# Kernel optimization log

Measured on AMD Instinct MI355X. Metric: run time of the kernel, lower is better.

Reference implementation:

```python
import jax, jax.numpy as jnp
import numpy as np

H, D = 8, 8          # num_heads, hidden_size (head dim)
SCALE = 0.25         # Hopfield beta/scaling
STEPS = 3            # update_steps_max
LN_EPS = 1e-5


def ln(x, g, b):
    m = x.mean(-1, keepdims=True)
    v = ((x - m) ** 2).mean(-1, keepdims=True)
    return (x - m) * jax.lax.rsqrt(v + LN_EPS) * g + b


def setup_inputs() -> dict:
    key = jax.random.key(0)
    ks = jax.random.split(key, 8)
    B, N, E = 32, 512, 512
    P = H * D  # 64 virtual hopfield dim
    s = lambda k, shape: jax.random.normal(k, shape, jnp.float32) * 0.05
    return dict(
        x=jax.random.normal(ks[0], (B, N, E), jnp.float32),
        g_q=jnp.ones((E,), jnp.float32), b_q=jnp.zeros((E,), jnp.float32),
        g_k=jnp.ones((E,), jnp.float32), b_k=jnp.zeros((E,), jnp.float32),
        g_v=jnp.ones((E,), jnp.float32), b_v=jnp.zeros((E,), jnp.float32),
        Wq=s(ks[1], (P, E)), bq=jnp.zeros((P,), jnp.float32),
        Wk=s(ks[2], (P, E)), bk=jnp.zeros((P,), jnp.float32),
        Wv=s(ks[3], (P, E)), bv=jnp.zeros((P,), jnp.float32),
        Wo=s(ks[4], (E, P)), bo=jnp.zeros((E,), jnp.float32),
        Wl=s(ks[5], (1, N * E)), bl=jnp.zeros((1,), jnp.float32),
    )


def reference(x, g_q, b_q, g_k, b_k, g_v, b_v,
              Wq, bq, Wk, bk, Wv, bv, Wo, bo, Wl, bl):
    B, N, E = x.shape
    # LayerNorm on state (query), stored (key), projection (value) patterns
    q = (ln(x, g_q, b_q) @ Wq.T + bq).reshape(B, N, H, D)
    k = (ln(x, g_k, b_k) @ Wk.T + bk).reshape(B, N, H, D)
    v = (ln(x, g_v, b_v) @ Wv.T + bv).reshape(B, N, H, D)
    # iterative Hopfield retrieval: xi <- softmax(beta * xi K^T) K
    xi = q
    for _ in range(STEPS):
        a = jax.nn.softmax(SCALE * jnp.einsum('bihd,bjhd->bhij', xi, k), axis=-1)
        xi = jnp.einsum('bhij,bjhd->bihd', a, k)
    # final association with value patterns
    a = jax.nn.softmax(SCALE * jnp.einsum('bihd,bjhd->bhij', xi, k), axis=-1)
    o = jnp.einsum('bhij,bjhd->bihd', a, v).reshape(B, N, H * D)
    o = o @ Wo.T + bo              # (B, N, E) out projection
    y = o.reshape(B, N * E) @ Wl.T + bl  # (B, 1) classifier head
    return y.reshape(-1)           # flatten(start_dim=0) -> (B,)
```

## Files before the change

### kernel.cpp

```cpp
#include <hip/hip_runtime.h>

#define E_DIM 512
#define N_DIM 512
#define B_DIM 32
#define H_DIM 8
#define D_DIM 8
#define P3    192

typedef _Float16 half_t;
typedef __attribute__((ext_vector_type(2))) _Float16 half2v;
typedef __attribute__((ext_vector_type(4))) _Float16 half4v;
typedef __attribute__((ext_vector_type(8))) _Float16 half8v;
typedef __attribute__((ext_vector_type(4))) float f32x4;
typedef __attribute__((ext_vector_type(16))) float f32x16;
typedef __attribute__((ext_vector_type(2))) unsigned int u32x2;
typedef __attribute__((ext_vector_type(4))) unsigned int u32x4;

#define XS_STRIDE 520
#define CQ 0.3606737602222409f
#define LS_RS 136

#define SM_KT0 0
#define SM_VT0 4608
#define SM_KB0 9216
#define SM_TOT 13312

__device__ inline float block_reduce_256(float v) {
    __shared__ float red[4];
    #pragma unroll
    for (int m = 32; m >= 1; m >>= 1) v += __shfl_xor(v, m);
    int w = threadIdx.x >> 6;
    if ((threadIdx.x & 63) == 0) red[w] = v;
    __syncthreads();
    if (threadIdx.x == 0) v = red[0] + red[1] + red[2] + red[3];
    return v;
}

__device__ inline half8v cvt8(float4 a, float4 b) {
    half8v h;
    h[0] = (half_t)a.x; h[1] = (half_t)a.y; h[2] = (half_t)a.z; h[3] = (half_t)a.w;
    h[4] = (half_t)b.x; h[5] = (half_t)b.y; h[6] = (half_t)b.z; h[7] = (half_t)b.w;
    return h;
}

__device__ inline unsigned pku(float a, float b) {
    return __builtin_bit_cast(unsigned, __builtin_amdgcn_cvt_pkrtz(a, b));
}

__device__ inline void plswap(unsigned &a, unsigned &b) {
    u32x2 r = __builtin_amdgcn_permlane32_swap(a, b, false, false);
    a = r[0]; b = r[1];
}

__device__ inline float bcast_lo(float v) {
    unsigned u = __builtin_bit_cast(unsigned, v);
    u32x2 r = __builtin_amdgcn_permlane32_swap(u, u, false, false);
    return __builtin_bit_cast(float, r[0]);
}

__global__ __launch_bounds__(256) void prep_w(const float* __restrict__ Wq,
                        const float* __restrict__ Wk, const float* __restrict__ Wv,
                        const float* __restrict__ gq, const float* __restrict__ gk,
                        const float* __restrict__ gv,
                        const float* __restrict__ bnq, const float* __restrict__ bnk,
                        const float* __restrict__ bnv,
                        const float* __restrict__ bq, const float* __restrict__ bk,
                        const float* __restrict__ bv,
                        const float* __restrict__ bl,
                        half_t* __restrict__ WthF, float* __restrict__ colsum,
                        float* __restrict__ b2, float* __restrict__ y,
                        float* __restrict__ c0acc) {
    int pp = blockIdx.x;
    int which = pp >> 6, p = pp & 63;
    int ct = pp >> 4, c16 = pp & 15;
    const float* W  = (which == 0) ? Wq  : (which == 1) ? Wk  : Wv;
    const float* g  = (which == 0) ? gq  : (which == 1) ? gk  : gv;
    const float* bn = (which == 0) ? bnq : (which == 1) ? bnk : bnv;
    const float* bb = (which == 0) ? bq  : (which == 1) ? bk  : bv;
    int t = threadIdx.x;
    if (pp == 0) {
        if (t < 32) y[t] = bl[0];
        if (t == 32) c0acc[0] = 0.f;
    }
    float cs = 0.f, dt = 0.f;
    #pragma unroll
    for (int l = 0; l < 2; ++l) {
        int e = t + l * 256;
        float wv = W[p * E_DIM + e];
        half_t wh = (half_t)(wv * g[e]);
        int k32 = e >> 5, g2 = (e >> 3) & 3, j = e & 7;
        WthF[(((size_t)(ct * 16 + k32) * 64) + g2 * 16 + c16) * 8 + j] = wh;
        cs += (float)wh;
        dt += wv * bn[e];
    }
    cs = block_reduce_256(cs);
    __syncthreads();
    dt = block_reduce_256(dt);
    if (t == 0) { colsum[pp] = cs; b2[pp] = dt + bb[p]; }
}

__global__ __launch_bounds__(256) void ln_qkv_wl2(const float* __restrict__ x,
                                              const half_t* __restrict__ WthF,
                                              const float* __restrict__ b2,
                                              const float* __restrict__ colsum,
                                              half_t* __restrict__ qkv16,
                                              const float* __restrict__ Wl,
                                              const float* __restrict__ Wo,
                                              const float* __restrict__ bo,
                                              float* __restrict__ Wl2,
                                              float* __restrict__ c0acc) {
    __shared__ half_t Xs[16 * XS_STRIDE];
    __shared__ half_t Ls[24 * LS_RS];
    __shared__ float stats[16][2];
    if (blockIdx.x < 1024) {
        const int t = threadIdx.x;
        const int lane = t & 63;
        const int w = t >> 6;
        const int g2 = lane >> 4, c16 = lane & 15;
        const int row0 = blockIdx.x * 16;
        {
            const int row = t >> 4, c = t & 15;
            const float4* xrow = (const float4*)(x + (size_t)(row0 + row) * E_DIM);
            float sx = 0.f, sxx = 0.f;
            #pragma unroll
            for (int l = 0; l < 8; ++l) {
                int f4 = c + l * 16;
                float4 a = xrow[f4];
                sx  += a.x + a.y + a.z + a.w;
                sxx += a.x*a.x + a.y*a.y + a.z*a.z + a.w*a.w;
                half4v h;
                h[0] = (half_t)a.x; h[1] = (half_t)a.y;
                h[2] = (half_t)a.z; h[3] = (half_t)a.w;
                *(half4v*)&Xs[row * XS_STRIDE + f4 * 4] = h;
            }
            #pragma unroll
            for (int m = 1; m <= 8; m <<= 1) {
                sx += __shfl_xor(sx, m); sxx += __shfl_xor(sxx, m);
            }
            if (c == 0) {
                float mean = sx * (1.f / E_DIM);
                float var  = sxx * (1.f / E_DIM) - mean * mean;
                stats[row][0] = mean;
                stats[row][1] = rsqrtf(var + 1e-5f);
            }
        }
        __syncthreads();
        f32x4 acc[3] = {{0.f,0.f,0.f,0.f},{0.f,0.f,0.f,0.f},{0.f,0.f,0.f,0.f}};
        const half_t* wf = WthF + (size_t)w * 3 * 16 * 512;
        #pragma unroll 4
        for (int k32 = 0; k32 < 16; ++k32) {
            half8v af = *(const half8v*)&Xs[c16 * XS_STRIDE + k32 * 32 + g2 * 8];
            #pragma unroll
            for (int nt = 0; nt < 3; ++nt) {
                half8v bf = *(const half8v*)(wf + ((size_t)(nt * 16 + k32)) * 512 + lane * 8);
                acc[nt] = __builtin_amdgcn_mfma_f32_16x16x32_f16(af, bf, acc[nt], 0, 0, 0);
            }
        }
        #pragma unroll
        for (int nt = 0; nt < 3; ++nt) {
            int pp = w * 48 + nt * 16 + c16;
            float cs = colsum[pp], bb = b2[pp];
            float qsc = (pp < 64) ? CQ : 1.0f;
            int region = pp >> 3, d = pp & 7;
            #pragma unroll
            for (int r = 0; r < 4; ++r) {
                int rowi = g2 * 4 + r;
                float val = (stats[rowi][1] * (acc[nt][r] - stats[rowi][0] * cs) + bb) * qsc;
                Ls[region * LS_RS + rowi * 8 + d] = (half_t)val;
            }
        }
        __syncthreads();
        const int b = row0 >> 9, n0 = row0 & 511;
        #pragma unroll
        for (int l = 0; l < 3; ++l) {
            int c = t + l * 256;
            int region = c >> 5, off = (c & 31) * 4;
            int which = region >> 3, h = region & 7;
            half4v v = *(const half4v*)&Ls[region * LS_RS + off];
            half_t* dst0 = qkv16 + (size_t)which * (B_DIM * H_DIM * N_DIM * D_DIM);
            int rowi = off >> 3, d0 = off & 7;
            *(half4v*)&dst0[(((size_t)(b * H_DIM + h)) * N_DIM + n0 + rowi) * D_DIM + d0] = v;
        }
    } else {
        const int blk = blockIdx.x - 1024;
        const int t = threadIdx.x;
        const int lane = t & 63;
        const int w = t >> 6;
        const int g2 = lane >> 4, c16 = lane & 15;
        const int n0 = blk * 16;
        const int pcol = w * 16;
        f32x4 acc = {0.f, 0.f, 0.f, 0.f};
        float pc = 0.f;
        const float* arow = Wl + (size_t)(n0 + c16) * E_DIM;
        #pragma unroll 2
        for (int k0 = 0; k0 < E_DIM; k0 += 32) {
            int kbase = k0 + g2 * 8;
            float4 a0 = *(const float4*)(arow + kbase);
            float4 a1 = *(const float4*)(arow + kbase + 4);
            if (w == 0) {
                float4 b0 = *(const float4*)(bo + kbase);
                float4 b1 = *(const float4*)(bo + kbase + 4);
                pc += a0.x*b0.x + a0.y*b0.y + a0.z*b0.z + a0.w*b0.w
                    + a1.x*b1.x + a1.y*b1.y + a1.z*b1.z + a1.w*b1.w;
            }
            half8v af = cvt8(a0, a1);
            half8v bf;
            #pragma unroll
            for (int j = 0; j < 8; ++j)
                bf[j] = (half_t)Wo[(size_t)(kbase + j) * 64 + pcol + c16];
            acc = __builtin_amdgcn_mfma_f32_16x16x32_f16(af, bf, acc, 0, 0, 0);
        }
        int p = pcol + c16, h = p >> 3, d = p & 7;
        #pragma unroll
        for (int r = 0; r < 4; ++r) {
            int n = n0 + g2 * 4 + r;
            Wl2[h * (N_DIM * D_DIM) + n * D_DIM + d] = acc[r];
        }
        if (w == 0) {
            pc += __shfl_xor(pc, 16); pc += __shfl_xor(pc, 32);
            pc += __shfl_xor(pc, 1);  pc += __shfl_xor(pc, 2);
            pc += __shfl_xor(pc, 4);  pc += __shfl_xor(pc, 8);
            if (lane == 0) atomicAdd(c0acc, pc);
        }
    }
}

__global__ __launch_bounds__(256, 4) void hopfield(const half_t* __restrict__ q16,
                                                   const half_t* __restrict__ k16,
                                                   const half_t* __restrict__ v16,
                                                   const float* __restrict__ Wl2,
                                                   const float* __restrict__ c0acc,
                                                   float* __restrict__ y) {
    __shared__ __align__(16) half_t sm[SM_TOT];
    const int t = threadIdx.x;
    const int lane = t & 63;
    const int w = t >> 6;
    const int lq = lane & 31;
    const int hi = lane >> 5;
    const int bh = blockIdx.x >> 2, seg = blockIdx.x & 3;
    const half_t* kg = k16 + (size_t)bh * (N_DIM * D_DIM);
    const half_t* vg = v16 + (size_t)bh * (N_DIM * D_DIM);
    const half_t* qg = q16 + (size_t)bh * (N_DIM * D_DIM) + seg * 128 * 8;
    const float* wl2p = Wl2 + (bh & 7) * (N_DIM * D_DIM) + seg * 128 * 8;

    {
        const int j0 = 2 * t;
        half8v r0 = *(const half8v*)(kg + j0 * 8);
        half8v r1 = *(const half8v*)(kg + j0 * 8 + 8);
        half8v v0 = *(const half8v*)(vg + j0 * 8);
        half8v v1 = *(const half8v*)(vg + j0 * 8 + 8);
        *(half8v*)&sm[SM_KB0 + j0 * 8]     = r0;
        *(half8v*)&sm[SM_KB0 + j0 * 8 + 8] = r1;
        const int kt = t >> 2, jp = j0 & 7;
        half_t* kb = &sm[SM_KT0 + kt * 72 + jp];
        half_t* vb = &sm[SM_VT0 + kt * 72 + jp];
        #pragma unroll
        for (int d = 0; d < 8; ++d) {
            half2v pk_; pk_[0] = r0[d]; pk_[1] = r1[d];
            *(half2v*)(kb + d * 8) = pk_;
            half2v pv_; pv_[0] = v0[d]; pv_[1] = v1[d];
            *(half2v*)(vb + d * 8) = pv_;
        }
        half2v one2; one2[0] = (half_t)1.f; one2[1] = (half_t)1.f;
        *(half2v*)(kb + 64) = one2;
        *(half2v*)(vb + 64) = one2;
    }
    __syncthreads();

    const half_t* akb = sm + SM_KB0 + lq * 8;
    int rowc = lq & 15; if (rowc > 8) rowc = 8;
    const half_t* aTk = sm + SM_KT0 + hi * 72 + rowc * 8;
    const half_t* aVk = sm + SM_VT0 + hi * 72 + rowc * 8;
    const f32x16 Zf16 = {};
    float fsum = 0.f;

    half8v bx;
    {
        half8v bq = *(const half8v*)(qg + (w * 32 + lq) * 8);
        u32x4 qw = __builtin_bit_cast(u32x4, bq);
        if (hi) { qw[0] = 0u; qw[1] = 0u; qw[2] = 0u; qw[3] = 0u; }
        bx = __builtin_bit_cast(half8v, qw);
    }

    for (int it = 0; it < 4; ++it) {
        const half_t* aTit = (it == 3) ? aVk : aTk;
        f32x16 U = {};
        half8v ak0 = *(const half8v*)akb;
        f32x16 Sn = __builtin_amdgcn_mfma_f32_32x32x16_f16(ak0, bx, Zf16, 0, 0, 0);
        #pragma unroll 4
        for (int tile = 0; tile < 16; ++tile) {
            f32x16 S = Sn;
            if (tile < 15) {
                half8v akn = *(const half8v*)(akb + (tile + 1) * 256);
                Sn = __builtin_amdgcn_mfma_f32_32x32x16_f16(akn, bx, Zf16, 0, 0, 0);
            }
            half8v aT0 = *(const half8v*)(aTit + tile * 288);
            half8v aT1 = *(const half8v*)(aTit + tile * 288 + 144);
            __builtin_amdgcn_s_setprio(1);
            unsigned wa = pku(__builtin_amdgcn_exp2f(S[0]),  __builtin_amdgcn_exp2f(S[1]));
            unsigned wb = pku(__builtin_amdgcn_exp2f(S[2]),  __builtin_amdgcn_exp2f(S[3]));
            unsigned wc = pku(__builtin_amdgcn_exp2f(S[4]),  __builtin_amdgcn_exp2f(S[5]));
            unsigned wd = pku(__builtin_amdgcn_exp2f(S[6]),  __builtin_amdgcn_exp2f(S[7]));
            unsigned we = pku(__builtin_amdgcn_exp2f(S[8]),  __builtin_amdgcn_exp2f(S[9]));
            unsigned wf = pku(__builtin_amdgcn_exp2f(S[10]), __builtin_amdgcn_exp2f(S[11]));
            unsigned wg = pku(__builtin_amdgcn_exp2f(S[12]), __builtin_amdgcn_exp2f(S[13]));
            unsigned wh = pku(__builtin_amdgcn_exp2f(S[14]), __builtin_amdgcn_exp2f(S[15]));
            plswap(wa, wc); plswap(wb, wd);
            plswap(we, wg); plswap(wf, wh);
            u32x4 c0 = {wa, wb, wc, wd};
            u32x4 c1 = {we, wf, wg, wh};
            U = __builtin_amdgcn_mfma_f32_32x32x16_f16(aT0, __builtin_bit_cast(half8v, c0), U, 0, 0, 0);
            U = __builtin_amdgcn_mfma_f32_32x32x16_f16(aT1, __builtin_bit_cast(half8v, c1), U, 0, 0, 0);
            __builtin_amdgcn_s_setprio(0);
        }
        float inv = __builtin_amdgcn_rcpf(bcast_lo(U[4]));
        if (it < 3) {
            float ci = CQ * inv;
            unsigned W01 = pku(U[0] * ci, U[1] * ci);
            unsigned W23 = pku(U[2] * ci, U[3] * ci);
            unsigned z1 = 0u, z2 = 0u;
            plswap(W01, z1);
            plswap(W23, z2);
            u32x4 nb = {W01, W23, z1, z2};
            bx = __builtin_bit_cast(half8v, nb);
        } else {
            float4 wv = *(const float4*)&wl2p[(w * 32 + lq) * 8 + hi * 4];
            fsum = inv * (U[0] * wv.x + U[1] * wv.y + U[2] * wv.z + U[3] * wv.w);
        }
    }
    float tot = block_reduce_256(fsum);
    if (t == 0) atomicAdd(&y[bh >> 3], tot);
    if (blockIdx.x == 0 && t < 32) {
        atomicAdd(&y[t], c0acc[0]);
    }
}

extern "C" void kernel_launch(void* const* d_in, const int* in_sizes, int n_in,
                              void* d_out, int out_size, void* d_ws, size_t ws_size,
                              hipStream_t stream) {
    const float* x   = (const float*)d_in[0];
    const float* g_q = (const float*)d_in[1];
    const float* b_q = (const float*)d_in[2];
    const float* g_k = (const float*)d_in[3];
    const float* b_k = (const float*)d_in[4];
    const float* g_v = (const float*)d_in[5];
    const float* b_v = (const float*)d_in[6];
    const float* Wq  = (const float*)d_in[7];
    const float* bq  = (const float*)d_in[8];
    const float* Wk  = (const float*)d_in[9];
    const float* bk  = (const float*)d_in[10];
    const float* Wv  = (const float*)d_in[11];
    const float* bv  = (const float*)d_in[12];
    const float* Wo  = (const float*)d_in[13];
    const float* bo  = (const float*)d_in[14];
    const float* Wl  = (const float*)d_in[15];
    const float* bl  = (const float*)d_in[16];
    float* out = (float*)d_out;

    float* ws = (float*)d_ws;
    float*  colsum = ws;
    float*  b2     = ws + 192;
    float*  c0acc  = ws + 384;
    float*  Wl2    = ws + 448;
    half_t* WthF   = (half_t*)(ws + 33216);
    half_t* qkv16  = (half_t*)(ws + 82368);

    half_t* q16 = qkv16;
    half_t* k16 = qkv16 + 1048576;
    half_t* v16 = qkv16 + 2097152;

    prep_w    <<<192, 256, 0, stream>>>(Wq, Wk, Wv, g_q, g_k, g_v,
                                        b_q, b_k, b_v, bq, bk, bv, bl,
                                        WthF, colsum, b2, out, c0acc);
    ln_qkv_wl2<<<1056, 256, 0, stream>>>(x, WthF, b2, colsum, qkv16,
                                         Wl, Wo, bo, Wl2, c0acc);
    hopfield  <<<1024, 256, 0, stream>>>(q16, k16, v16, Wl2, c0acc, out);
}
```

Baseline: 155.6 us.

## Process two query tiles per wave in hopfield and prefetch first weight fragments

The hopfield kernel now handles 256 queries per block instead of 128, giving each wave two independent 32-query tiles that share the same K/V LDS fragments and interleave two MFMA/exp chains. This halves the block count and the per-block K/V staging into shared memory, and gives more independent instruction streams to hide MFMA latency, at the cost of more registers and fewer blocks to fill the GPU. Separately, the first k-step weight fragments in the LN/QKV kernel are loaded before the LayerNorm statistics pass so their global latency overlaps it.

```diff
diff --git a/kernel.cpp b/kernel.cpp
--- a/kernel.cpp
+++ b/kernel.cpp
@@ -118,6 +118,10 @@
         const int w = t >> 6;
         const int g2 = lane >> 4, c16 = lane & 15;
         const int row0 = blockIdx.x * 16;
+        const half_t* wf = WthF + (size_t)w * 3 * 16 * 512;
+        half8v pb0 = *(const half8v*)(wf + (size_t)( 0) * 512 + lane * 8);
+        half8v pb1 = *(const half8v*)(wf + (size_t)(16) * 512 + lane * 8);
+        half8v pb2 = *(const half8v*)(wf + (size_t)(32) * 512 + lane * 8);
         {
             const int row = t >> 4, c = t & 15;
             const float4* xrow = (const float4*)(x + (size_t)(row0 + row) * E_DIM);
@@ -146,9 +150,14 @@
         }
         __syncthreads();
         f32x4 acc[3] = {{0.f,0.f,0.f,0.f},{0.f,0.f,0.f,0.f},{0.f,0.f,0.f,0.f}};
-        const half_t* wf = WthF + (size_t)w * 3 * 16 * 512;
-        #pragma unroll 4
-        for (int k32 = 0; k32 < 16; ++k32) {
+        {
+            half8v af = *(const half8v*)&Xs[c16 * XS_STRIDE + g2 * 8];
+            acc[0] = __builtin_amdgcn_mfma_f32_16x16x32_f16(af, pb0, acc[0], 0, 0, 0);
+            acc[1] = __builtin_amdgcn_mfma_f32_16x16x32_f16(af, pb1, acc[1], 0, 0, 0);
+            acc[2] = __builtin_amdgcn_mfma_f32_16x16x32_f16(af, pb2, acc[2], 0, 0, 0);
+        }
+        #pragma unroll 5
+        for (int k32 = 1; k32 < 16; ++k32) {
             half8v af = *(const half8v*)&Xs[c16 * XS_STRIDE + k32 * 32 + g2 * 8];
             #pragma unroll
             for (int nt = 0; nt < 3; ++nt) {
@@ -237,11 +246,11 @@
     const int w = t >> 6;
     const int lq = lane & 31;
     const int hi = lane >> 5;
-    const int bh = blockIdx.x >> 2, seg = blockIdx.x & 3;
+    const int bh = blockIdx.x >> 1, seg = blockIdx.x & 1;
     const half_t* kg = k16 + (size_t)bh * (N_DIM * D_DIM);
     const half_t* vg = v16 + (size_t)bh * (N_DIM * D_DIM);
-    const half_t* qg = q16 + (size_t)bh * (N_DIM * D_DIM) + seg * 128 * 8;
-    const float* wl2p = Wl2 + (bh & 7) * (N_DIM * D_DIM) + seg * 128 * 8;
+    const half_t* qg = q16 + (size_t)bh * (N_DIM * D_DIM) + seg * 256 * 8;
+    const float* wl2p = Wl2 + (bh & 7) * (N_DIM * D_DIM) + seg * 256 * 8;
 
     {
         const int j0 = 2 * t;
@@ -274,58 +283,89 @@
     const f32x16 Zf16 = {};
     float fsum = 0.f;
 
-    half8v bx;
+    half8v bxA, bxB;
     {
-        half8v bq = *(const half8v*)(qg + (w * 32 + lq) * 8);
-        u32x4 qw = __builtin_bit_cast(u32x4, bq);
-        if (hi) { qw[0] = 0u; qw[1] = 0u; qw[2] = 0u; qw[3] = 0u; }
-        bx = __builtin_bit_cast(half8v, qw);
+        half8v qa = *(const half8v*)(qg + (w * 64 + lq) * 8);
+        half8v qb = *(const half8v*)(qg + (w * 64 + 32 + lq) * 8);
+        u32x4 wa = __builtin_bit_cast(u32x4, qa);
+        u32x4 wb = __builtin_bit_cast(u32x4, qb);
+        if (hi) {
+            wa[0] = 0u; wa[1] = 0u; wa[2] = 0u; wa[3] = 0u;
+            wb[0] = 0u; wb[1] = 0u; wb[2] = 0u; wb[3] = 0u;
+        }
+        bxA = __builtin_bit_cast(half8v, wa);
+        bxB = __builtin_bit_cast(half8v, wb);
     }
 
     for (int it = 0; it < 4; ++it) {
         const half_t* aTit = (it == 3) ? aVk : aTk;
-        f32x16 U = {};
-        half8v ak0 = *(const half8v*)akb;
-        f32x16 Sn = __builtin_amdgcn_mfma_f32_32x32x16_f16(ak0, bx, Zf16, 0, 0, 0);
+        f32x16 UA = {}, UB = {};
         #pragma unroll 4
         for (int tile = 0; tile < 16; ++tile) {
-            f32x16 S = Sn;
-            if (tile < 15) {
-                half8v akn = *(const half8v*)(akb + (tile + 1) * 256);
-                Sn = __builtin_amdgcn_mfma_f32_32x32x16_f16(akn, bx, Zf16, 0, 0, 0);
-            }
+            half8v ak  = *(const half8v*)(akb + tile * 256);
             half8v aT0 = *(const half8v*)(aTit + tile * 288);
             half8v aT1 = *(const half8v*)(aTit + tile * 288 + 144);
+            f32x16 SA = __builtin_amdgcn_mfma_f32_32x32x16_f16(ak, bxA, Zf16, 0, 0, 0);
+            f32x16 SB = __builtin_amdgcn_mfma_f32_32x32x16_f16(ak, bxB, Zf16, 0, 0, 0);
             __builtin_amdgcn_s_setprio(1);
-            unsigned wa = pku(__builtin_amdgcn_exp2f(S[0]),  __builtin_amdgcn_exp2f(S[1]));
-            unsigned wb = pku(__builtin_amdgcn_exp2f(S[2]),  __builtin_amdgcn_exp2f(S[3]));
-            unsigned wc = pku(__builtin_amdgcn_exp2f(S[4]),  __builtin_amdgcn_exp2f(S[5]));
-            unsigned wd = pku(__builtin_amdgcn_exp2f(S[6]),  __builtin_amdgcn_exp2f(S[7]));
-            unsigned we = pku(__builtin_amdgcn_exp2f(S[8]),  __builtin_amdgcn_exp2f(S[9]));
-            unsigned wf = pku(__builtin_amdgcn_exp2f(S[10]), __builtin_amdgcn_exp2f(S[11]));
-            unsigned wg = pku(__builtin_amdgcn_exp2f(S[12]), __builtin_amdgcn_exp2f(S[13]));
-            unsigned wh = pku(__builtin_amdgcn_exp2f(S[14]), __builtin_amdgcn_exp2f(S[15]));
-            plswap(wa, wc); plswap(wb, wd);
-            plswap(we, wg); plswap(wf, wh);
-            u32x4 c0 = {wa, wb, wc, wd};
-            u32x4 c1 = {we, wf, wg, wh};
-            U = __builtin_amdgcn_mfma_f32_32x32x16_f16(aT0, __builtin_bit_cast(half8v, c0), U, 0, 0, 0);
-            U = __builtin_amdgcn_mfma_f32_32x32x16_f16(aT1, __builtin_bit_cast(half8v, c1), U, 0, 0, 0);
+            {
+                unsigned wa = pku(__builtin_amdgcn_exp2f(SA[0]),  __builtin_amdgcn_exp2f(SA[1]));
+                unsigned wb = pku(__builtin_amdgcn_exp2f(SA[2]),  __builtin_amdgcn_exp2f(SA[3]));
+                unsigned wc = pku(__builtin_amdgcn_exp2f(SA[4]),  __builtin_amdgcn_exp2f(SA[5]));
+                unsigned wd = pku(__builtin_amdgcn_exp2f(SA[6]),  __builtin_amdgcn_exp2f(SA[7]));
+                unsigned we = pku(__builtin_amdgcn_exp2f(SA[8]),  __builtin_amdgcn_exp2f(SA[9]));
+                unsigned wf = pku(__builtin_amdgcn_exp2f(SA[10]), __builtin_amdgcn_exp2f(SA[11]));
+                unsigned wg = pku(__builtin_amdgcn_exp2f(SA[12]), __builtin_amdgcn_exp2f(SA[13]));
+                unsigned wh = pku(__builtin_amdgcn_exp2f(SA[14]), __builtin_amdgcn_exp2f(SA[15]));
+                plswap(wa, wc); plswap(wb, wd);
+                plswap(we, wg); plswap(wf, wh);
+                u32x4 c0 = {wa, wb, wc, wd};
+                u32x4 c1 = {we, wf, wg, wh};
+                UA = __builtin_amdgcn_mfma_f32_32x32x16_f16(aT0, __builtin_bit_cast(half8v, c0), UA, 0, 0, 0);
+                UA = __builtin_amdgcn_mfma_f32_32x32x16_f16(aT1, __builtin_bit_cast(half8v, c1), UA, 0, 0, 0);
+            }
+            {
+                unsigned wa = pku(__builtin_amdgcn_exp2f(SB[0]),  __builtin_amdgcn_exp2f(SB[1]));
+                unsigned wb = pku(__builtin_amdgcn_exp2f(SB[2]),  __builtin_amdgcn_exp2f(SB[3]));
+                unsigned wc = pku(__builtin_amdgcn_exp2f(SB[4]),  __builtin_amdgcn_exp2f(SB[5]));
+                unsigned wd = pku(__builtin_amdgcn_exp2f(SB[6]),  __builtin_amdgcn_exp2f(SB[7]));
+                unsigned we = pku(__builtin_amdgcn_exp2f(SB[8]),  __builtin_amdgcn_exp2f(SB[9]));
+                unsigned wf = pku(__builtin_amdgcn_exp2f(SB[10]), __builtin_amdgcn_exp2f(SB[11]));
+                unsigned wg = pku(__builtin_amdgcn_exp2f(SB[12]), __builtin_amdgcn_exp2f(SB[13]));
+                unsigned wh = pku(__builtin_amdgcn_exp2f(SB[14]), __builtin_amdgcn_exp2f(SB[15]));
+                plswap(wa, wc); plswap(wb, wd);
+                plswap(we, wg); plswap(wf, wh);
+                u32x4 c0 = {wa, wb, wc, wd};
+                u32x4 c1 = {we, wf, wg, wh};
+                UB = __builtin_amdgcn_mfma_f32_32x32x16_f16(aT0, __builtin_bit_cast(half8v, c0), UB, 0, 0, 0);
+                UB = __builtin_amdgcn_mfma_f32_32x32x16_f16(aT1, __builtin_bit_cast(half8v, c1), UB, 0, 0, 0);
+            }
             __builtin_amdgcn_s_setprio(0);
         }
-        float inv = __builtin_amdgcn_rcpf(bcast_lo(U[4]));
+        float invA = __builtin_amdgcn_rcpf(bcast_lo(UA[4]));
+        float invB = __builtin_amdgcn_rcpf(bcast_lo(UB[4]));
         if (it < 3) {
-            float ci = CQ * inv;
-            unsigned W01 = pku(U[0] * ci, U[1] * ci);
-            unsigned W23 = pku(U[2] * ci, U[3] * ci);
-            unsigned z1 = 0u, z2 = 0u;
-            plswap(W01, z1);
-            plswap(W23, z2);
-            u32x4 nb = {W01, W23, z1, z2};
-            bx = __builtin_bit_cast(half8v, nb);
+            float ciA = CQ * invA;
+            unsigned A01 = pku(UA[0] * ciA, UA[1] * ciA);
+            unsigned A23 = pku(UA[2] * ciA, UA[3] * ciA);
+            unsigned za1 = 0u, za2 = 0u;
+            plswap(A01, za1);
+            plswap(A23, za2);
+            u32x4 na = {A01, A23, za1, za2};
+            bxA = __builtin_bit_cast(half8v, na);
+            float ciB = CQ * invB;
+            unsigned B01 = pku(UB[0] * ciB, UB[1] * ciB);
+            unsigned B23 = pku(UB[2] * ciB, UB[3] * ciB);
+            unsigned zb1 = 0u, zb2 = 0u;
+            plswap(B01, zb1);
+            plswap(B23, zb2);
+            u32x4 nb = {B01, B23, zb1, zb2};
+            bxB = __builtin_bit_cast(half8v, nb);
         } else {
-            float4 wv = *(const float4*)&wl2p[(w * 32 + lq) * 8 + hi * 4];
-            fsum = inv * (U[0] * wv.x + U[1] * wv.y + U[2] * wv.z + U[3] * wv.w);
+            float4 wva = *(const float4*)&wl2p[(w * 64 + lq) * 8 + hi * 4];
+            float4 wvb = *(const float4*)&wl2p[(w * 64 + 32 + lq) * 8 + hi * 4];
+            fsum = invA * (UA[0] * wva.x + UA[1] * wva.y + UA[2] * wva.z + UA[3] * wva.w)
+                 + invB * (UB[0] * wvb.x + UB[1] * wvb.y + UB[2] * wvb.z + UB[3] * wvb.w);
         }
     }
     float tot = block_reduce_256(fsum);
@@ -374,5 +414,5 @@
                                         WthF, colsum, b2, out, c0acc);
     ln_qkv_wl2<<<1056, 256, 0, stream>>>(x, WthF, b2, colsum, qkv16,
                                          Wl, Wo, bo, Wl2, c0acc);
-    hopfield  <<<1024, 256, 0, stream>>>(q16, k16, v16, Wl2, c0acc, out);
-}
+    hopfield  <<<512, 256, 0, stream>>>(q16, k16, v16, Wl2, c0acc, out);
+}
```

After: 152.1 us. -2.2%, faster.
